# Kernel tuning notes

Measured on AMD Instinct MI355X. Metric: run time of the kernel, lower is better.

Reference implementation:

```python
import jax, jax.numpy as jnp
import numpy as np
from jax import lax

B = 64
FEAT = 512
SEED_DIM = 128
NUM_PC = 256
NPART = 4096
NFPS = 512


def setup_inputs() -> dict:
    key = jax.random.key(0)
    ks = jax.random.split(key, 32)
    s = 0.02
    rn = lambda k, shape: jax.random.normal(k, shape, jnp.float32) * s
    inp = {}
    inp["feat"] = jax.random.normal(ks[0], (B, FEAT, 1), jnp.float32)
    inp["patch_xyz"] = jax.random.normal(ks[1], (B, 3, 128), jnp.float32)
    inp["patch_feat"] = jax.random.normal(ks[2], (B, FEAT, 128), jnp.float32)
    inp["partial"] = jax.random.normal(ks[3], (B, NPART, 3), jnp.float32)
    # ConvTranspose1d(512, 128, 256): weight [in, out, k]
    inp["ps_w"] = rn(ks[4], (FEAT, 128, NUM_PC))
    inp["ps_b"] = jnp.zeros((128,), jnp.float32)
    # MLP_Res(in, hidden, out): conv1 [hid,in], conv2 [out,hid], shortcut [out,in]
    def mlp_res_params(k, din, dhid, dout):
        k1, k2, k3 = jax.random.split(k, 3)
        return (rn(k1, (dhid, din)), jnp.zeros((dhid,), jnp.float32),
                rn(k2, (dout, dhid)), jnp.zeros((dout,), jnp.float32),
                rn(k3, (dout, din)), jnp.zeros((dout,), jnp.float32))
    (inp["m1_w1"], inp["m1_b1"], inp["m1_w2"], inp["m1_b2"], inp["m1_ws"], inp["m1_bs"]) = mlp_res_params(ks[5], FEAT + 128, 128, 128)
    (inp["m2_w1"], inp["m2_b1"], inp["m2_w2"], inp["m2_b2"], inp["m2_ws"], inp["m2_bs"]) = mlp_res_params(ks[6], 128, 64, 128)
    (inp["m3_w1"], inp["m3_b1"], inp["m3_w2"], inp["m3_b2"], inp["m3_ws"], inp["m3_bs"]) = mlp_res_params(ks[7], FEAT + 128, 128, SEED_DIM)
    inp["m4_w1"] = rn(ks[8], (64, SEED_DIM))
    inp["m4_b1"] = jnp.zeros((64,), jnp.float32)
    inp["m4_w2"] = rn(ks[9], (3, 64))
    inp["m4_b2"] = jnp.zeros((3,), jnp.float32)
    return inp


def _conv1(w, b, x):
    # 1x1 Conv1d: w [out,in], x [B,in,N] -> [B,out,N]
    return jnp.einsum('oi,bin->bon', w, x) + b[None, :, None]


def _mlp_res(x, w1, b1, w2, b2, ws, bs):
    h = jax.nn.relu(_conv1(w1, b1, x))
    return _conv1(w2, b2, h) + _conv1(ws, bs, x)


def _fps(xyz, npoint):
    # farthest point sampling (PointNet++ semantics, start at index 0)
    # xyz: [B, N, 3] -> [B, npoint, 3]
    Bb, N, _ = xyz.shape
    dist0 = jnp.full((Bb, N), 1e10, dtype=xyz.dtype)
    far0 = jnp.zeros((Bb,), jnp.int32)

    def step(carry, _):
        dist, far = carry
        centroid = jnp.take_along_axis(xyz, far[:, None, None], axis=1)  # [B,1,3]
        d = jnp.sum((xyz - centroid) ** 2, axis=-1)  # [B,N]
        dist = jnp.minimum(dist, d)
        new_far = jnp.argmax(dist, axis=-1).astype(jnp.int32)
        return (dist, new_far), far

    _, idxs = lax.scan(step, (dist0, far0), None, length=npoint)  # [npoint, B]
    idxs = idxs.T  # [B, npoint]
    return jnp.take_along_axis(xyz, idxs[..., None], axis=1)


def reference(feat, patch_xyz, patch_feat, partial,
              ps_w, ps_b,
              m1_w1, m1_b1, m1_w2, m1_b2, m1_ws, m1_bs,
              m2_w1, m2_b1, m2_w2, m2_b2, m2_ws, m2_bs,
              m3_w1, m3_b1, m3_w2, m3_b2, m3_ws, m3_bs,
              m4_w1, m4_b1, m4_w2, m4_b2):
    # ConvTranspose1d on length-1 input: [B,C,1] x [C,O,K] -> [B,O,K]
    x1 = jnp.einsum('bc,cok->bok', feat[:, :, 0], ps_w) + ps_b[None, :, None]
    feat_r = jnp.broadcast_to(feat, (feat.shape[0], feat.shape[1], NUM_PC))
    x1 = _mlp_res(jnp.concatenate([x1, feat_r], axis=1), m1_w1, m1_b1, m1_w2, m1_b2, m1_ws, m1_bs)
    x2 = _mlp_res(x1, m2_w1, m2_b1, m2_w2, m2_b2, m2_ws, m2_bs)
    x3 = _mlp_res(jnp.concatenate([x2, feat_r], axis=1), m3_w1, m3_b1, m3_w2, m3_b2, m3_ws, m3_bs)
    seed = _conv1(m4_w2, m4_b2, jax.nn.relu(_conv1(m4_w1, m4_b1, x3)))  # [B,3,256]
    all_pts = jnp.concatenate([seed.transpose(0, 2, 1), partial], axis=1)  # [B,256+N,3]
    x = _fps(all_pts, NFPS).transpose(0, 2, 1)  # [B,3,512]
    return (seed, x3, x)
```

## Files before the change

### kernel.cpp

```cpp
#include <hip/hip_runtime.h>
#include <stdint.h>

#define X3_OFF 49152
#define FPS_OFF 2146304


__global__ void k_prep(const float* __restrict__ feat, float* __restrict__ ws) {
    int g = blockIdx.x * 256 + threadIdx.x;
    int c = g >> 6, b = g & 63;
    ws[32768 + c * 64 + b] = feat[b * 512 + c];
}

__global__ void k_tterms(const float* __restrict__ w1, const float* __restrict__ ws1,
                         const float* __restrict__ w3, const float* __restrict__ ws3,
                         float* __restrict__ ws) {
    int g = blockIdx.x * 256 + threadIdx.x;
    int which = g >> 13;
    int o = (g >> 6) & 127;
    int b = g & 63;
    const float* W = (which == 0) ? w1 : (which == 1) ? ws1
                     : (which == 2) ? w3 : ws3;
    const float* ft = ws + 32768;
    float acc = 0.f;
    for (int c = 0; c < 512; ++c)
        acc = fmaf(W[o * 640 + 128 + c], ft[c * 64 + b], acc);
    ws[which * 8192 + o * 64 + b] = acc;
}

__global__ void k_deconv(const float* __restrict__ psw,
                         const float* __restrict__ psb,
                         const float* __restrict__ ws,
                         float* __restrict__ stage) {
    int n = blockIdx.x * 256 + threadIdx.x;
    int b0 = blockIdx.y * 16;
    const float* featT = ws + 32768;
    float acc[16];
    float bias = psb[n >> 8];
#pragma unroll
    for (int j = 0; j < 16; ++j) acc[j] = bias;
    for (int c = 0; c < 512; ++c) {
        float pw = psw[c * 32768 + n];
#pragma unroll
        for (int j = 0; j < 16; ++j)
            acc[j] = fmaf(pw, featT[c * 64 + b0 + j], acc[j]);
    }
#pragma unroll
    for (int j = 0; j < 16; ++j)
        stage[(b0 + j) * 32768 + n] = acc[j];
}

__device__ __forceinline__ void gemm8(const float* __restrict__ Wg, int ld, int o0,
                                      const float* S, int K, float acc[8], int lane) {
#pragma unroll 4
    for (int i = 0; i < K; ++i) {
        float x = S[i * 64 + lane];
#pragma unroll
        for (int r = 0; r < 8; ++r)
            acc[r] = fmaf(x, Wg[(o0 + r) * ld + i], acc[r]);
    }
}

struct FusedW {
    const float *m1_w1, *m1_b1, *m1_w2, *m1_b2, *m1_ws, *m1_bs;
    const float *m2_w1, *m2_b1, *m2_w2, *m2_b2, *m2_ws, *m2_bs;
    const float *m3_w1, *m3_b1, *m3_w2, *m3_b2, *m3_ws, *m3_bs;
    const float *m4_w1, *m4_b1, *m4_w2, *m4_b2;
};

__global__ void __launch_bounds__(512)
k_fused(FusedW P, const float* __restrict__ ws, float* __restrict__ fout) {
    int b  = blockIdx.x >> 2;
    int k0 = (blockIdx.x & 3) * 64;
    int lane = threadIdx.x & 63;
    int wave = __builtin_amdgcn_readfirstlane(threadIdx.x >> 6);

    const float* T1  = ws;
    const float* T1s = ws + 8192;
    const float* T3  = ws + 16384;
    const float* T3s = ws + 24576;
    float* stage = fout + X3_OFF + b * 32768;

    __shared__ float Xs[8192];
    __shared__ float Hs[8192];

#pragma unroll
    for (int s = 0; s < 16; ++s) {
        int e = threadIdx.x + s * 512;
        int o = e >> 6, kk = e & 63;
        Xs[e] = stage[o * 256 + k0 + kk];
    }
    __syncthreads();

    float yreg[2][8];

#pragma unroll
    for (int half = 0; half < 2; ++half) {
        int o0 = wave * 16 + half * 8;
        float acc[8];
#pragma unroll
        for (int r = 0; r < 8; ++r) acc[r] = T1[(o0 + r) * 64 + b] + P.m1_b1[o0 + r];
        gemm8(P.m1_w1, 640, o0, Xs, 128, acc, lane);
#pragma unroll
        for (int r = 0; r < 8; ++r) Hs[(o0 + r) * 64 + lane] = fmaxf(acc[r], 0.f);
    }
    __syncthreads();
#pragma unroll
    for (int half = 0; half < 2; ++half) {
        int o0 = wave * 16 + half * 8;
        float acc[8];
#pragma unroll
        for (int r = 0; r < 8; ++r)
            acc[r] = T1s[(o0 + r) * 64 + b] + P.m1_b2[o0 + r] + P.m1_bs[o0 + r];
        gemm8(P.m1_w2, 128, o0, Hs, 128, acc, lane);
        gemm8(P.m1_ws, 640, o0, Xs, 128, acc, lane);
#pragma unroll
        for (int r = 0; r < 8; ++r) yreg[half][r] = acc[r];
    }
    __syncthreads();
#pragma unroll
    for (int half = 0; half < 2; ++half) {
        int o0 = wave * 16 + half * 8;
#pragma unroll
        for (int r = 0; r < 8; ++r) Xs[(o0 + r) * 64 + lane] = yreg[half][r];
    }
    __syncthreads();

    {
        int o0 = wave * 8;
        float acc[8];
#pragma unroll
        for (int r = 0; r < 8; ++r) acc[r] = P.m2_b1[o0 + r];
        gemm8(P.m2_w1, 128, o0, Xs, 128, acc, lane);
#pragma unroll
        for (int r = 0; r < 8; ++r) Hs[(o0 + r) * 64 + lane] = fmaxf(acc[r], 0.f);
    }
    __syncthreads();
#pragma unroll
    for (int half = 0; half < 2; ++half) {
        int o0 = wave * 16 + half * 8;
        float acc[8];
#pragma unroll
        for (int r = 0; r < 8; ++r) acc[r] = P.m2_b2[o0 + r] + P.m2_bs[o0 + r];
        gemm8(P.m2_w2, 64, o0, Hs, 64, acc, lane);
        gemm8(P.m2_ws, 128, o0, Xs, 128, acc, lane);
#pragma unroll
        for (int r = 0; r < 8; ++r) yreg[half][r] = acc[r];
    }
    __syncthreads();
#pragma unroll
    for (int half = 0; half < 2; ++half) {
        int o0 = wave * 16 + half * 8;
#pragma unroll
        for (int r = 0; r < 8; ++r) Xs[(o0 + r) * 64 + lane] = yreg[half][r];
    }
    __syncthreads();

#pragma unroll
    for (int half = 0; half < 2; ++half) {
        int o0 = wave * 16 + half * 8;
        float acc[8];
#pragma unroll
        for (int r = 0; r < 8; ++r) acc[r] = T3[(o0 + r) * 64 + b] + P.m3_b1[o0 + r];
        gemm8(P.m3_w1, 640, o0, Xs, 128, acc, lane);
#pragma unroll
        for (int r = 0; r < 8; ++r) Hs[(o0 + r) * 64 + lane] = fmaxf(acc[r], 0.f);
    }
    __syncthreads();
#pragma unroll
    for (int half = 0; half < 2; ++half) {
        int o0 = wave * 16 + half * 8;
        float acc[8];
#pragma unroll
        for (int r = 0; r < 8; ++r)
            acc[r] = T3s[(o0 + r) * 64 + b] + P.m3_b2[o0 + r] + P.m3_bs[o0 + r];
        gemm8(P.m3_w2, 128, o0, Hs, 128, acc, lane);
        gemm8(P.m3_ws, 640, o0, Xs, 128, acc, lane);
#pragma unroll
        for (int r = 0; r < 8; ++r) yreg[half][r] = acc[r];
    }
    __syncthreads();
#pragma unroll
    for (int half = 0; half < 2; ++half) {
        int o0 = wave * 16 + half * 8;
#pragma unroll
        for (int r = 0; r < 8; ++r) {
            Xs[(o0 + r) * 64 + lane] = yreg[half][r];
            stage[(o0 + r) * 256 + k0 + lane] = yreg[half][r];
        }
    }
    __syncthreads();

    {
        int o0 = wave * 8;
        float acc[8];
#pragma unroll
        for (int r = 0; r < 8; ++r) acc[r] = P.m4_b1[o0 + r];
        gemm8(P.m4_w1, 128, o0, Xs, 128, acc, lane);
#pragma unroll
        for (int r = 0; r < 8; ++r) Hs[(o0 + r) * 64 + lane] = fmaxf(acc[r], 0.f);
    }
    __syncthreads();
    if (wave < 3) {
        int d = wave;
        float s = P.m4_b2[d];
        for (int j = 0; j < 64; ++j)
            s = fmaf(Hs[j * 64 + lane], P.m4_w2[d * 64 + j], s);
        fout[b * 768 + d * 256 + k0 + lane] = s;
    }
}

__device__ __forceinline__ unsigned wave_max_u32_l63(unsigned v) {
    unsigned t;
    t = (unsigned)__builtin_amdgcn_update_dpp(0, (int)v, 0x111, 0xf, 0xf, false); v = t > v ? t : v;
    t = (unsigned)__builtin_amdgcn_update_dpp(0, (int)v, 0x112, 0xf, 0xf, false); v = t > v ? t : v;
    t = (unsigned)__builtin_amdgcn_update_dpp(0, (int)v, 0x114, 0xf, 0xf, false); v = t > v ? t : v;
    t = (unsigned)__builtin_amdgcn_update_dpp(0, (int)v, 0x118, 0xf, 0xf, false); v = t > v ? t : v;
    t = (unsigned)__builtin_amdgcn_update_dpp(0, (int)v, 0x142, 0xa, 0xf, false); v = t > v ? t : v;
    t = (unsigned)__builtin_amdgcn_update_dpp(0, (int)v, 0x143, 0xc, 0xf, false); v = t > v ? t : v;
    return v;
}
__device__ __forceinline__ unsigned wave_min_u32_l63(unsigned v) {
    unsigned t;
    t = (unsigned)__builtin_amdgcn_update_dpp(-1, (int)v, 0x111, 0xf, 0xf, false); v = t < v ? t : v;
    t = (unsigned)__builtin_amdgcn_update_dpp(-1, (int)v, 0x112, 0xf, 0xf, false); v = t < v ? t : v;
    t = (unsigned)__builtin_amdgcn_update_dpp(-1, (int)v, 0x114, 0xf, 0xf, false); v = t < v ? t : v;
    t = (unsigned)__builtin_amdgcn_update_dpp(-1, (int)v, 0x118, 0xf, 0xf, false); v = t < v ? t : v;
    t = (unsigned)__builtin_amdgcn_update_dpp(-1, (int)v, 0x142, 0xa, 0xf, false); v = t < v ? t : v;
    t = (unsigned)__builtin_amdgcn_update_dpp(-1, (int)v, 0x143, 0xc, 0xf, false); v = t < v ? t : v;
    return v;
}

__global__ void __launch_bounds__(256)
k_fps(const float* __restrict__ seed, const float* __restrict__ partial,
      float* __restrict__ outx) {
    int b = blockIdx.x;
    int tid = threadIdx.x;
    int lane = tid & 63;
    int wv = tid >> 6;

    __shared__ float pts[4352 * 3];
    __shared__ unsigned long long cand[2][4];
    __shared__ int fars[512];

    pts[tid * 3 + 0] = seed[b * 768 + tid];
    pts[tid * 3 + 1] = seed[b * 768 + 256 + tid];
    pts[tid * 3 + 2] = seed[b * 768 + 512 + tid];
#pragma unroll
    for (int j = 0; j < 48; ++j) {
        int e = tid + j * 256;
        pts[768 + e] = partial[b * 12288 + e];
    }
    if (tid == 0) fars[0] = 0;
    __syncthreads();

    float px[17], py[17], pz[17], dist[17];
#pragma unroll
    for (int s = 0; s < 17; ++s) {
        int g = s * 256 + tid;
        px[s] = pts[g * 3 + 0];
        py[s] = pts[g * 3 + 1];
        pz[s] = pts[g * 3 + 2];
        dist[s] = 1e10f;
    }
    float cx = pts[0], cy = pts[1], cz = pts[2];

    for (int t = 0; t < 511; ++t) {
        float bv = -1.0f; int bg = 0;
#pragma unroll
        for (int s = 0; s < 17; ++s) {
            float dx = px[s] - cx, dy = py[s] - cy, dz = pz[s] - cz;
            float d = __fadd_rn(__fadd_rn(__fmul_rn(dx, dx), __fmul_rn(dy, dy)),
                                __fmul_rn(dz, dz));
            dist[s] = fminf(dist[s], d);
            if (dist[s] > bv) { bv = dist[s]; bg = s * 256 + tid; }
        }
        unsigned mv = wave_max_u32_l63(__float_as_uint(bv));
        unsigned maxbits = (unsigned)__builtin_amdgcn_readlane((int)mv, 63);
        unsigned cg = (__float_as_uint(bv) == maxbits) ? (unsigned)bg : 0xFFFFFFFFu;
        unsigned mgv = wave_min_u32_l63(cg);
        unsigned big = (unsigned)__builtin_amdgcn_readlane((int)mgv, 63);

        if (lane == 0)
            cand[t & 1][wv] = (((unsigned long long)maxbits) << 32) |
                              (unsigned long long)(8191u - big);
        __syncthreads();
        unsigned long long U0 = cand[t & 1][0];
        unsigned long long U1 = cand[t & 1][1];
        unsigned long long U2 = cand[t & 1][2];
        unsigned long long U3 = cand[t & 1][3];
        if (U1 > U0) U0 = U1;
        if (U3 > U2) U2 = U3;
        if (U2 > U0) U0 = U2;
        int bi = 8191 - (int)(U0 & 8191ull);
        cx = pts[bi * 3 + 0]; cy = pts[bi * 3 + 1]; cz = pts[bi * 3 + 2];
        if (tid == 0) fars[t + 1] = bi;
    }
    __syncthreads();

#pragma unroll
    for (int j = 0; j < 2; ++j) {
        int n = tid + j * 256;
        int idx = fars[n];
        int ob = b * 1536 + n;
        outx[ob]        = pts[idx * 3 + 0];
        outx[ob + 512]  = pts[idx * 3 + 1];
        outx[ob + 1024] = pts[idx * 3 + 2];
    }
}

extern "C" void kernel_launch(void* const* d_in, const int* in_sizes, int n_in,
                              void* d_out, int out_size, void* d_ws, size_t ws_size,
                              hipStream_t stream) {
    (void)in_sizes; (void)n_in; (void)out_size; (void)ws_size;
    const float* feat    = (const float*)d_in[0];
    const float* partial = (const float*)d_in[3];
    const float* psw     = (const float*)d_in[4];
    const float* psb     = (const float*)d_in[5];

    FusedW P;
    P.m1_w1 = (const float*)d_in[6];  P.m1_b1 = (const float*)d_in[7];
    P.m1_w2 = (const float*)d_in[8];  P.m1_b2 = (const float*)d_in[9];
    P.m1_ws = (const float*)d_in[10]; P.m1_bs = (const float*)d_in[11];
    P.m2_w1 = (const float*)d_in[12]; P.m2_b1 = (const float*)d_in[13];
    P.m2_w2 = (const float*)d_in[14]; P.m2_b2 = (const float*)d_in[15];
    P.m2_ws = (const float*)d_in[16]; P.m2_bs = (const float*)d_in[17];
    P.m3_w1 = (const float*)d_in[18]; P.m3_b1 = (const float*)d_in[19];
    P.m3_w2 = (const float*)d_in[20]; P.m3_b2 = (const float*)d_in[21];
    P.m3_ws = (const float*)d_in[22]; P.m3_bs = (const float*)d_in[23];
    P.m4_w1 = (const float*)d_in[24]; P.m4_b1 = (const float*)d_in[25];
    P.m4_w2 = (const float*)d_in[26]; P.m4_b2 = (const float*)d_in[27];

    float* W = (float*)d_ws;
    float* out = (float*)d_out;

    k_prep<<<dim3(128), dim3(256), 0, stream>>>(feat, W);
    k_tterms<<<dim3(128), dim3(256), 0, stream>>>(P.m1_w1, P.m1_ws, P.m3_w1, P.m3_ws, W);
    k_deconv<<<dim3(128, 4), dim3(256), 0, stream>>>(psw, psb, W, out + X3_OFF);
    k_fused<<<dim3(256), dim3(512), 0, stream>>>(P, W, out);
    k_fps<<<dim3(64), dim3(256), 0, stream>>>(out, partial, out + FPS_OFF);
}
```

Baseline: 729.9 us.

## Pack FPS distance math into float2, widen deconv batch tile, scalarize gemm row index

The FPS loop now keeps points in two-wide float vectors so the distance subtract, multiply and add can map to packed FP32 instructions, which should shorten the serial 511-step critical path. The deconv kernel gives each thread 32 batches instead of 16 and launches half as many blocks, so every ps_w load is reused twice as often, at the cost of more registers and fewer blocks. gemm8 marks its row offset as wave-uniform with readfirstlane so the weight addressing can go through scalar registers. Packed arithmetic may fuse multiply-add differently from the explicit round-to-nearest ops, so FPS distance ties could change.

Measured after the change: 832.9 us. 14.1% more time.

```diff
diff --git a/kernel.cpp b/kernel.cpp
--- a/kernel.cpp
+++ b/kernel.cpp
@@ -3,6 +3,8 @@
 
 #define X3_OFF 49152
 #define FPS_OFF 2146304
+
+typedef float v2f __attribute__((ext_vector_type(2)));
 
 
 __global__ void k_prep(const float* __restrict__ feat, float* __restrict__ ws) {
@@ -27,30 +29,32 @@
     ws[which * 8192 + o * 64 + b] = acc;
 }
 
-__global__ void k_deconv(const float* __restrict__ psw,
-                         const float* __restrict__ psb,
-                         const float* __restrict__ ws,
-                         float* __restrict__ stage) {
+__global__ void __launch_bounds__(256, 2)
+k_deconv(const float* __restrict__ psw,
+         const float* __restrict__ psb,
+         const float* __restrict__ ws,
+         float* __restrict__ stage) {
     int n = blockIdx.x * 256 + threadIdx.x;
-    int b0 = blockIdx.y * 16;
+    int b0 = blockIdx.y * 32;
     const float* featT = ws + 32768;
-    float acc[16];
+    float acc[32];
     float bias = psb[n >> 8];
 #pragma unroll
-    for (int j = 0; j < 16; ++j) acc[j] = bias;
+    for (int j = 0; j < 32; ++j) acc[j] = bias;
     for (int c = 0; c < 512; ++c) {
         float pw = psw[c * 32768 + n];
 #pragma unroll
-        for (int j = 0; j < 16; ++j)
+        for (int j = 0; j < 32; ++j)
             acc[j] = fmaf(pw, featT[c * 64 + b0 + j], acc[j]);
     }
 #pragma unroll
-    for (int j = 0; j < 16; ++j)
+    for (int j = 0; j < 32; ++j)
         stage[(b0 + j) * 32768 + n] = acc[j];
 }
 
 __device__ __forceinline__ void gemm8(const float* __restrict__ Wg, int ld, int o0,
                                       const float* S, int K, float acc[8], int lane) {
+    o0 = __builtin_amdgcn_readfirstlane(o0);
 #pragma unroll 4
     for (int i = 0; i < K; ++i) {
         float x = S[i * 64 + lane];
@@ -253,26 +257,41 @@
     if (tid == 0) fars[0] = 0;
     __syncthreads();
 
-    float px[17], py[17], pz[17], dist[17];
-#pragma unroll
-    for (int s = 0; s < 17; ++s) {
-        int g = s * 256 + tid;
-        px[s] = pts[g * 3 + 0];
-        py[s] = pts[g * 3 + 1];
-        pz[s] = pts[g * 3 + 2];
-        dist[s] = 1e10f;
+    v2f px[9], py[9], pz[9], dist[9];
+#pragma unroll
+    for (int j = 0; j < 9; ++j) {
+        int g0 = (2 * j) * 256 + tid;
+        px[j].x = pts[g0 * 3 + 0];
+        py[j].x = pts[g0 * 3 + 1];
+        pz[j].x = pts[g0 * 3 + 2];
+        dist[j].x = 1e10f;
+        if (j < 8) {
+            int g1 = (2 * j + 1) * 256 + tid;
+            px[j].y = pts[g1 * 3 + 0];
+            py[j].y = pts[g1 * 3 + 1];
+            pz[j].y = pts[g1 * 3 + 2];
+            dist[j].y = 1e10f;
+        } else {
+            px[j].y = 0.f; py[j].y = 0.f; pz[j].y = 0.f;
+            dist[j].y = -1.0f;
+        }
     }
     float cx = pts[0], cy = pts[1], cz = pts[2];
 
     for (int t = 0; t < 511; ++t) {
+        v2f c2x = {cx, cx}, c2y = {cy, cy}, c2z = {cz, cz};
         float bv = -1.0f; int bg = 0;
 #pragma unroll
-        for (int s = 0; s < 17; ++s) {
-            float dx = px[s] - cx, dy = py[s] - cy, dz = pz[s] - cz;
-            float d = __fadd_rn(__fadd_rn(__fmul_rn(dx, dx), __fmul_rn(dy, dy)),
-                                __fmul_rn(dz, dz));
-            dist[s] = fminf(dist[s], d);
-            if (dist[s] > bv) { bv = dist[s]; bg = s * 256 + tid; }
+        for (int j = 0; j < 9; ++j) {
+            v2f dx = px[j] - c2x;
+            v2f dy = py[j] - c2y;
+            v2f dz = pz[j] - c2z;
+            v2f d = (dx * dx + dy * dy) + dz * dz;
+            float d0 = fminf(dist[j].x, d.x);
+            float d1 = fminf(dist[j].y, d.y);
+            dist[j].x = d0; dist[j].y = d1;
+            if (d0 > bv) { bv = d0; bg = (2 * j) * 256 + tid; }
+            if (d1 > bv) { bv = d1; bg = (2 * j + 1) * 256 + tid; }
         }
         unsigned mv = wave_max_u32_l63(__float_as_uint(bv));
         unsigned maxbits = (unsigned)__builtin_amdgcn_readlane((int)mv, 63);
@@ -335,7 +354,7 @@
 
     k_prep<<<dim3(128), dim3(256), 0, stream>>>(feat, W);
     k_tterms<<<dim3(128), dim3(256), 0, stream>>>(P.m1_w1, P.m1_ws, P.m3_w1, P.m3_ws, W);
-    k_deconv<<<dim3(128, 4), dim3(256), 0, stream>>>(psw, psb, W, out + X3_OFF);
+    k_deconv<<<dim3(128, 2), dim3(256), 0, stream>>>(psw, psb, W, out + X3_OFF);
     k_fused<<<dim3(256), dim3(512), 0, stream>>>(P, W, out);
     k_fps<<<dim3(64), dim3(256), 0, stream>>>(out, partial, out + FPS_OFF);
 }
```
